# Kernel tuning notes

Hardware: AMD Instinct MI355X
Metric: run time of the kernel (lower is better)

## Reference

```python
import jax, jax.numpy as jnp
import numpy as np

D_MODEL = 1024
N_HEAD = 16
D_HEAD = D_MODEL // N_HEAD


def setup_inputs() -> dict:
    key = jax.random.key(0)
    k_x, k_wqkv, k_bqkv, k_wp, k_bp = jax.random.split(key, 5)
    B, T = 2, 2048
    bound = 1.0 / np.sqrt(D_MODEL)
    return {
        "x": jax.random.normal(k_x, (B, T, D_MODEL), dtype=jnp.float32),
        "w_qkv": jax.random.uniform(k_wqkv, (D_MODEL, 3 * D_MODEL), jnp.float32, -bound, bound),
        "b_qkv": jax.random.uniform(k_bqkv, (3 * D_MODEL,), jnp.float32, -bound, bound),
        "w_proj": jax.random.uniform(k_wp, (D_MODEL, D_MODEL), jnp.float32, -bound, bound),
        "b_proj": jax.random.uniform(k_bp, (D_MODEL,), jnp.float32, -bound, bound),
    }


def reference(x, w_qkv, b_qkv, w_proj, b_proj):
    B, T, C = x.shape
    qkv = x @ w_qkv + b_qkv                       # [B,T,3C]
    qkv = qkv.reshape(B, T, 3, N_HEAD, D_HEAD)
    qkv = jnp.transpose(qkv, (2, 0, 3, 1, 4))      # [3,B,H,T,dh]
    q, k, v = qkv[0], qkv[1], qkv[2]
    scale = np.sqrt(D_HEAD).astype(np.float32)
    attn = jnp.einsum("bhqd,bhkd->bhqk", q, k) / scale  # [B,H,T,T]
    causal = jnp.tril(jnp.ones((T, T), dtype=bool))
    attn = jnp.where(causal, attn, -jnp.inf)
    attn = jax.nn.softmax(attn, axis=-1)
    out = jnp.einsum("bhqk,bhkd->bhqd", attn, v)   # [B,H,T,dh]
    out = jnp.transpose(out, (0, 2, 1, 3)).reshape(B, T, C)
    return out @ w_proj + b_proj
```

## Files before the change

### kernel.cpp

```cpp
#include <hip/hip_runtime.h>
#include <hip/hip_bf16.h>
#include <math.h>

constexpr int Bb   = 2;
constexpr int T    = 2048;
constexpr int C    = 1024;
constexpr int H    = 16;
constexpr int M    = Bb * T;
constexpr int NQKV = 3 * C;

typedef __attribute__((ext_vector_type(8))) short bf16x8;
typedef __attribute__((ext_vector_type(4))) float f32x4;

__device__ inline short f2bf(float f) {
    __hip_bfloat16 h = __float2bfloat16(f);
    return *reinterpret_cast<short*>(&h);
}

#if __has_builtin(__builtin_amdgcn_exp2f)
#define EXP2(x) __builtin_amdgcn_exp2f(x)
#else
#define EXP2(x) exp2f(x)
#endif

#define GLOBAL_AS __attribute__((address_space(1)))
#define LDS_AS    __attribute__((address_space(3)))

__device__ __forceinline__ void gload_lds16(const short* g, short* s) {
    __builtin_amdgcn_global_load_lds((const GLOBAL_AS void*)g, (LDS_AS void*)s, 16, 0, 0);
}

__global__ __launch_bounds__(256)
void prep_all(const float* __restrict__ x, short* __restrict__ xb,
              const float* __restrict__ w_qkv, short* __restrict__ wqkvt,
              const float* __restrict__ w_proj, short* __restrict__ wprojt)
{
    __shared__ float tile[32][33];
    const int blk = blockIdx.x;
    const int tid = threadIdx.x;

    if (blk < 4096) {
        const int i = blk * 1024 + tid * 4;
        const float4 v = *(const float4*)(x + i);
        short4 s;
        s.x = f2bf(v.x); s.y = f2bf(v.y); s.z = f2bf(v.z); s.w = f2bf(v.w);
        *(short4*)(xb + i) = s;
        return;
    }

    const bool isqkv = (blk < 7168);
    const int bidx = isqkv ? (blk - 4096) : (blk - 7168);
    const int nblk = isqkv ? 96 : 32;
    const int N    = isqkv ? NQKV : C;
    const float* W = isqkv ? w_qkv : w_proj;
    short* Wt      = isqkv ? wqkvt : wprojt;

    const int n0 = (bidx % nblk) * 32, k0 = (bidx / nblk) * 32;
    const int tx = tid & 31, ty = tid >> 5;
#pragma unroll
    for (int i = 0; i < 32; i += 8)
        tile[ty + i][tx] = W[(size_t)(k0 + ty + i) * N + n0 + tx];
    __syncthreads();
#pragma unroll
    for (int i = 0; i < 32; i += 8)
        Wt[(size_t)(n0 + ty + i) * C + k0 + tx] = f2bf(tile[tx][ty + i]);
}

__global__ __launch_bounds__(256)
void gemm_mfma(const short* __restrict__ A, const short* __restrict__ Bt,
               const float* __restrict__ bias, short* __restrict__ outp,
               int Ndim, int Kdim)
{
    __shared__ __align__(16) short As[2 * 128 * 32];
    __shared__ __align__(16) short Bs[2 * 128 * 32];

    const int tid = threadIdx.x;
    const int w   = tid >> 6;
    const int l   = tid & 63;
    const int lk  = l & 15;
    const int lq  = l >> 4;

    const int gx  = gridDim.x;
    const int nwg = gx * gridDim.y;
    const int cpx = nwg >> 3;
    const int bid = blockIdx.y * gx + blockIdx.x;
    const int swz = (bid & 7) * cpx + (bid >> 3);
    const int m0  = (swz / gx) * 128;
    const int n0  = (swz % gx) * 128;

    const int mw  = (w >> 1) * 64, nw = (w & 1) * 64;

    const int srow = w * 16 + (l >> 2);
    const int scol = (l & 3) * 8;

    const short* agp0 = A  + (size_t)(m0 + srow)      * Kdim + scol;
    const short* agp1 = A  + (size_t)(m0 + 64 + srow) * Kdim + scol;
    const short* bgp0 = Bt + (size_t)(n0 + srow)      * Kdim + scol;
    const short* bgp1 = Bt + (size_t)(n0 + 64 + srow) * Kdim + scol;

    short* ad0 = &As[w * 512];
    short* ad1 = &As[2048 + w * 512];
    short* bd0 = &Bs[w * 512];
    short* bd1 = &Bs[2048 + w * 512];

    f32x4 acc[4][4];
#pragma unroll
    for (int i = 0; i < 4; ++i)
#pragma unroll
        for (int j = 0; j < 4; ++j) acc[i][j] = (f32x4){0.f, 0.f, 0.f, 0.f};

    gload_lds16(agp0, ad0);
    gload_lds16(agp1, ad1);
    gload_lds16(bgp0, bd0);
    gload_lds16(bgp1, bd1);
    __syncthreads();

    int cur = 0;
    for (int k0 = 0; k0 < Kdim; k0 += 32) {
        const int coff = cur ? 4096 : 0;

        bf16x8 af[4], bfr[4];
#pragma unroll
        for (int mt = 0; mt < 4; ++mt)
            af[mt] = *(const bf16x8*)&As[coff + (mw + mt * 16 + lk) * 32 + lq * 8];
#pragma unroll
        for (int nt = 0; nt < 4; ++nt)
            bfr[nt] = *(const bf16x8*)&Bs[coff + (nw + nt * 16 + lk) * 32 + lq * 8];

        if (k0 + 32 < Kdim) {
            const int noff = cur ? 0 : 4096;
            gload_lds16(agp0 + k0 + 32, ad0 + noff);
            gload_lds16(agp1 + k0 + 32, ad1 + noff);
            gload_lds16(bgp0 + k0 + 32, bd0 + noff);
            gload_lds16(bgp1 + k0 + 32, bd1 + noff);
        }

#pragma unroll
        for (int mt = 0; mt < 4; ++mt)
#pragma unroll
            for (int nt = 0; nt < 4; ++nt)
                acc[mt][nt] = __builtin_amdgcn_mfma_f32_16x16x32_bf16(bfr[nt], af[mt], acc[mt][nt], 0, 0, 0);

        __syncthreads();
        cur ^= 1;
    }

    float4 bv[4];
#pragma unroll
    for (int nt = 0; nt < 4; ++nt)
        bv[nt] = *(const float4*)(bias + n0 + nw + nt * 16 + lq * 4);
#pragma unroll
    for (int mt = 0; mt < 4; ++mt) {
        short* rowp = outp + (size_t)(m0 + mw + mt * 16 + lk) * Ndim + n0 + nw + lq * 4;
#pragma unroll
        for (int nt = 0; nt < 4; ++nt) {
            short4 pk;
            pk.x = f2bf(acc[mt][nt][0] + bv[nt].x);
            pk.y = f2bf(acc[mt][nt][1] + bv[nt].y);
            pk.z = f2bf(acc[mt][nt][2] + bv[nt].z);
            pk.w = f2bf(acc[mt][nt][3] + bv[nt].w);
            *(short4*)(rowp + nt * 16) = pk;
        }
    }
}

__global__ __launch_bounds__(256)
void gemm_mfma_proj(const short* __restrict__ A, const short* __restrict__ Bt,
                    const float* __restrict__ bias, float* __restrict__ outp,
                    int Ndim, int Kdim)
{
    __shared__ __align__(16) short As[2 * 64 * 32];
    __shared__ __align__(16) short Bs[2 * 128 * 32];

    const int tid = threadIdx.x;
    const int w   = tid >> 6;
    const int l   = tid & 63;
    const int lk  = l & 15;
    const int lq  = l >> 4;

    const int gx  = gridDim.x;
    const int nwg = gx * gridDim.y;
    const int cpx = nwg >> 3;
    const int bid = blockIdx.y * gx + blockIdx.x;
    const int swz = (bid & 7) * cpx + (bid >> 3);
    const int m0  = (swz / gx) * 64;
    const int n0  = (swz % gx) * 128;

    const int mw  = (w & 1) * 32, nw = (w >> 1) * 64;

    const int srow = w * 16 + (l >> 2);
    const int scol = (l & 3) * 8;

    const short* agp  = A  + (size_t)(m0 + srow)      * Kdim + scol;
    const short* bgp0 = Bt + (size_t)(n0 + srow)      * Kdim + scol;
    const short* bgp1 = Bt + (size_t)(n0 + 64 + srow) * Kdim + scol;

    short* ad  = &As[w * 512];
    short* bd0 = &Bs[w * 512];
    short* bd1 = &Bs[2048 + w * 512];

    f32x4 acc[2][4];
#pragma unroll
    for (int i = 0; i < 2; ++i)
#pragma unroll
        for (int j = 0; j < 4; ++j) acc[i][j] = (f32x4){0.f, 0.f, 0.f, 0.f};

    gload_lds16(agp,  ad);
    gload_lds16(bgp0, bd0);
    gload_lds16(bgp1, bd1);
    __syncthreads();

    int cur = 0;
    for (int k0 = 0; k0 < Kdim; k0 += 32) {
        const int coffA = cur ? 2048 : 0;
        const int coffB = cur ? 4096 : 0;

        bf16x8 af[2], bfr[4];
#pragma unroll
        for (int mt = 0; mt < 2; ++mt)
            af[mt] = *(const bf16x8*)&As[coffA + (mw + mt * 16 + lk) * 32 + lq * 8];
#pragma unroll
        for (int nt = 0; nt < 4; ++nt)
            bfr[nt] = *(const bf16x8*)&Bs[coffB + (nw + nt * 16 + lk) * 32 + lq * 8];

        if (k0 + 32 < Kdim) {
            const int noffA = cur ? 0 : 2048;
            const int noffB = cur ? 0 : 4096;
            gload_lds16(agp  + k0 + 32, ad  + noffA);
            gload_lds16(bgp0 + k0 + 32, bd0 + noffB);
            gload_lds16(bgp1 + k0 + 32, bd1 + noffB);
        }

#pragma unroll
        for (int mt = 0; mt < 2; ++mt)
#pragma unroll
            for (int nt = 0; nt < 4; ++nt)
                acc[mt][nt] = __builtin_amdgcn_mfma_f32_16x16x32_bf16(bfr[nt], af[mt], acc[mt][nt], 0, 0, 0);

        __syncthreads();
        cur ^= 1;
    }

    float4 bv[4];
#pragma unroll
    for (int nt = 0; nt < 4; ++nt)
        bv[nt] = *(const float4*)(bias + n0 + nw + nt * 16 + lq * 4);
#pragma unroll
    for (int mt = 0; mt < 2; ++mt) {
        float* rowp = outp + (size_t)(m0 + mw + mt * 16 + lk) * Ndim + n0 + nw + lq * 4;
#pragma unroll
        for (int nt = 0; nt < 4; ++nt) {
            float4 v;
            v.x = acc[mt][nt][0] + bv[nt].x;
            v.y = acc[mt][nt][1] + bv[nt].y;
            v.z = acc[mt][nt][2] + bv[nt].z;
            v.w = acc[mt][nt][3] + bv[nt].w;
            *(float4*)(rowp + nt * 16) = v;
        }
    }
}

constexpr int LDV = 136;
constexpr float SC = 0.18033688f;

__global__ __launch_bounds__(256, 4)
void attn_mfma(const short* __restrict__ qkv, short* __restrict__ att)
{
    __shared__ __align__(16) short Ks[128 * 64];
    __shared__ __align__(16) short Vt[64 * LDV];

    const int idx = blockIdx.x;
    const int xcd = idx & 7;
    const int j   = idx >> 3;
    const int bh  = xcd * 4 + (j & 3);
    const int s   = j >> 2;
    const int qt  = (s < 8)  ? (31 - s)
                  : (s < 16) ? (s - 8)
                  : (s < 24) ? (39 - s)
                  :            (s - 16);
    const int b   = bh >> 4;
    const int h   = bh & 15;
    const int qbase = qt * 64;

    const int tid = threadIdx.x;
    const int w   = tid >> 6;
    const int l   = tid & 63;
    const int lk  = l & 15;
    const int lq  = l >> 4;

    const short* base = qkv + (size_t)b * T * 3072 + h * 64;

    const int q_abs = qbase + w * 16 + lk;
    const short* qp = base + (size_t)q_abs * 3072 + lq * 8;
    const bf16x8 qf0 = *(const bf16x8*)qp;
    const bf16x8 qf1 = *(const bf16x8*)(qp + 32);

    f32x4 acc_o[4];
#pragma unroll
    for (int dt = 0; dt < 4; ++dt) acc_o[dt] = (f32x4){0.f, 0.f, 0.f, 0.f};
    float m_run = -INFINITY;
    float l_run = 0.f;

    const int krow   = l >> 3;
    const int kcolsw = 8 * ((l & 7) ^ (l >> 3));
    const int swz    = lk & 7;

    const int kg   = tid & 31;
    const int vd0  = (tid >> 5) * 8;
    const int pcol = ((kg & 24) | ((kg & 3) << 1) | ((kg >> 2) & 1)) * 4;

    const int nkt = (qbase + 64 + 127) >> 7;
#pragma unroll 1
    for (int it = 0; it < nkt; ++it) {
        const int j0 = it * 128;
        __syncthreads();
#pragma unroll
        for (int rr = 0; rr < 4; ++rr) {
            const int g = w * 32 + rr * 8;
            gload_lds16(base + 1024 + (size_t)(j0 + g + krow) * 3072 + kcolsw, &Ks[g * 64]);
        }
        {
            const short* vp = base + 2048 + (size_t)(j0 + kg * 4) * 3072 + vd0;
            bf16x8 vv[4];
#pragma unroll
            for (int kk = 0; kk < 4; ++kk)
                vv[kk] = *(const bf16x8*)(vp + (size_t)kk * 3072);
#pragma unroll
            for (int d = 0; d < 8; ++d) {
                short4 pk;
                pk.x = vv[0][d]; pk.y = vv[1][d]; pk.z = vv[2][d]; pk.w = vv[3][d];
                *(short4*)&Vt[(vd0 + d) * LDV + pcol] = pk;
            }
        }
        __syncthreads();

        f32x4 s4[8];
#pragma unroll
        for (int kt = 0; kt < 8; ++kt) {
            const int row = kt * 16 + lk;
            const bf16x8 kf0 = *(const bf16x8*)&Ks[row * 64 + 8 * (lq ^ swz)];
            const bf16x8 kf1 = *(const bf16x8*)&Ks[row * 64 + 8 * ((lq + 4) ^ swz)];
            f32x4 a = (f32x4){0.f, 0.f, 0.f, 0.f};
            a = __builtin_amdgcn_mfma_f32_16x16x32_bf16(kf0, qf0, a, 0, 0, 0);
            a = __builtin_amdgcn_mfma_f32_16x16x32_bf16(kf1, qf1, a, 0, 0, 0);
            s4[kt] = a;
        }

        if (it == nkt - 1) {
#pragma unroll
            for (int kt = 0; kt < 8; ++kt)
#pragma unroll
                for (int r = 0; r < 4; ++r)
                    if (j0 + kt * 16 + lq * 4 + r > q_abs) s4[kt][r] = -1e30f;
        }

        float mx = s4[0][0];
#pragma unroll
        for (int kt = 0; kt < 8; ++kt)
#pragma unroll
            for (int r = 0; r < 4; ++r) mx = fmaxf(mx, s4[kt][r]);
        mx = fmaxf(mx, __shfl_xor(mx, 16));
        mx = fmaxf(mx, __shfl_xor(mx, 32));
        const float mn   = fmaxf(m_run, mx);
        const float corr = EXP2((m_run - mn) * SC);
        m_run = mn;
        const float nmc = -mn * SC;
#pragma unroll
        for (int kt = 0; kt < 8; ++kt)
#pragma unroll
            for (int r = 0; r < 4; ++r)
                s4[kt][r] = EXP2(fmaf(s4[kt][r], SC, nmc));
        float ps = 0.f;
#pragma unroll
        for (int kt = 0; kt < 8; ++kt)
            ps += ((s4[kt][0] + s4[kt][1]) + (s4[kt][2] + s4[kt][3]));
        ps += __shfl_xor(ps, 16);
        ps += __shfl_xor(ps, 32);
        l_run = l_run * corr + ps;

        unsigned int d0[8], d1[8];
#pragma unroll
        for (int kt = 0; kt < 8; ++kt) {
            d0[kt] = (unsigned int)(unsigned short)f2bf(s4[kt][0])
                   | ((unsigned int)(unsigned short)f2bf(s4[kt][1]) << 16);
            d1[kt] = (unsigned int)(unsigned short)f2bf(s4[kt][2])
                   | ((unsigned int)(unsigned short)f2bf(s4[kt][3]) << 16);
        }

#pragma unroll
        for (int dt = 0; dt < 4; ++dt)
#pragma unroll
            for (int r = 0; r < 4; ++r) acc_o[dt][r] *= corr;

#pragma unroll
        for (int kc = 0; kc < 4; ++kc) {
            union { unsigned int u[4]; bf16x8 v; } up;
            up.u[0] = d0[kc * 2];
            up.u[1] = d1[kc * 2];
            up.u[2] = d0[kc * 2 + 1];
            up.u[3] = d1[kc * 2 + 1];
            const bf16x8 pf = up.v;
#pragma unroll
            for (int dt = 0; dt < 4; ++dt) {
                const bf16x8 vf = *(const bf16x8*)&Vt[(dt * 16 + lk) * LDV + kc * 32 + lq * 8];
                acc_o[dt] = __builtin_amdgcn_mfma_f32_16x16x32_bf16(vf, pf, acc_o[dt], 0, 0, 0);
            }
        }
    }

    const float inv = 1.f / l_run;
    short* op = att + ((size_t)(b * T + q_abs)) * 1024 + h * 64;
#pragma unroll
    for (int dt = 0; dt < 4; ++dt) {
        short4 pk;
        pk.x = f2bf(acc_o[dt][0] * inv);
        pk.y = f2bf(acc_o[dt][1] * inv);
        pk.z = f2bf(acc_o[dt][2] * inv);
        pk.w = f2bf(acc_o[dt][3] * inv);
        *(short4*)(op + dt * 16 + lq * 4) = pk;
    }
}

extern "C" void kernel_launch(void* const* d_in, const int* in_sizes, int n_in,
                              void* d_out, int out_size, void* d_ws, size_t ws_size,
                              hipStream_t stream)
{
    const float* x      = (const float*)d_in[0];
    const float* w_qkv  = (const float*)d_in[1];
    const float* b_qkv  = (const float*)d_in[2];
    const float* w_proj = (const float*)d_in[3];
    const float* b_proj = (const float*)d_in[4];
    float* out = (float*)d_out;

    short* xb     = (short*)d_ws;
    short* wqkvt  = xb     + (size_t)M * C;
    short* wprojt = wqkvt  + (size_t)NQKV * C;
    short* qkvb   = wprojt + (size_t)C * C;
    short* attb   = qkvb   + (size_t)M * NQKV;

    prep_all<<<8192, 256, 0, stream>>>(x, xb, w_qkv, wqkvt, w_proj, wprojt);
    gemm_mfma<<<dim3(NQKV / 128, M / 128), 256, 0, stream>>>(xb, wqkvt, b_qkv, qkvb, NQKV, C);
    attn_mfma<<<1024, 256, 0, stream>>>(qkvb, attb);
    gemm_mfma_proj<<<dim3(C / 128, M / 64), 256, 0, stream>>>(attb, wprojt, b_proj, out, C, C);
}
```

Measured before the change: 179.8 us.

## Double-buffer K/V tiles in attention with 512-thread blocks over 128-query tiles

The attention kernel now uses 512-thread blocks, each covering 128 queries, with double-buffered shared memory for K and transposed V. Warps 0-3 prefetch the next K tile through direct global-to-LDS loads, and warps 4-7 load the next V tile into registers and write it transposed after the PV MFMAs. The aim is to overlap global loads with compute, drop one barrier per iteration, and share each K/V tile across twice as many queries. In exchange, shared memory per block doubles and the grid halves to 512 blocks, which may lower occupancy and load balance under the causal mask.

```diff
diff --git a/kernel.cpp b/kernel.cpp
--- a/kernel.cpp
+++ b/kernel.cpp
@@ -263,24 +263,21 @@
 constexpr int LDV = 136;
 constexpr float SC = 0.18033688f;
 
-__global__ __launch_bounds__(256, 4)
+__global__ __launch_bounds__(512, 4)
 void attn_mfma(const short* __restrict__ qkv, short* __restrict__ att)
 {
-    __shared__ __align__(16) short Ks[128 * 64];
-    __shared__ __align__(16) short Vt[64 * LDV];
+    __shared__ __align__(16) short Ks[2][128 * 64];
+    __shared__ __align__(16) short Vt[2][64 * LDV];
 
     const int idx = blockIdx.x;
     const int xcd = idx & 7;
     const int j   = idx >> 3;
     const int bh  = xcd * 4 + (j & 3);
     const int s   = j >> 2;
-    const int qt  = (s < 8)  ? (31 - s)
-                  : (s < 16) ? (s - 8)
-                  : (s < 24) ? (39 - s)
-                  :            (s - 16);
+    const int qt  = (s < 8) ? s : (23 - s);
     const int b   = bh >> 4;
     const int h   = bh & 15;
-    const int qbase = qt * 64;
+    const int qbase = qt * 128;
 
     const int tid = threadIdx.x;
     const int w   = tid >> 6;
@@ -306,40 +303,62 @@
     const int swz    = lk & 7;
 
     const int kg   = tid & 31;
-    const int vd0  = (tid >> 5) * 8;
+    const int vd0  = ((tid >> 5) & 7) * 8;
     const int pcol = ((kg & 24) | ((kg & 3) << 1) | ((kg >> 2) & 1)) * 4;
 
-    const int nkt = (qbase + 64 + 127) >> 7;
+    const int nkt = qt + 1;
+
+    bf16x8 vv[4];
+
+    if (w < 4) {
+#pragma unroll
+        for (int rr = 0; rr < 4; ++rr) {
+            const int g = w * 32 + rr * 8;
+            gload_lds16(base + 1024 + (size_t)(g + krow) * 3072 + kcolsw, &Ks[0][g * 64]);
+        }
+    } else {
+        const short* vp = base + 2048 + (size_t)(kg * 4) * 3072 + vd0;
+#pragma unroll
+        for (int kk = 0; kk < 4; ++kk)
+            vv[kk] = *(const bf16x8*)(vp + (size_t)kk * 3072);
+#pragma unroll
+        for (int d = 0; d < 8; ++d) {
+            short4 pk;
+            pk.x = vv[0][d]; pk.y = vv[1][d]; pk.z = vv[2][d]; pk.w = vv[3][d];
+            *(short4*)&Vt[0][(vd0 + d) * LDV + pcol] = pk;
+        }
+    }
+    __syncthreads();
+
 #pragma unroll 1
     for (int it = 0; it < nkt; ++it) {
-        const int j0 = it * 128;
-        __syncthreads();
-#pragma unroll
-        for (int rr = 0; rr < 4; ++rr) {
-            const int g = w * 32 + rr * 8;
-            gload_lds16(base + 1024 + (size_t)(j0 + g + krow) * 3072 + kcolsw, &Ks[g * 64]);
-        }
-        {
-            const short* vp = base + 2048 + (size_t)(j0 + kg * 4) * 3072 + vd0;
-            bf16x8 vv[4];
-#pragma unroll
-            for (int kk = 0; kk < 4; ++kk)
-                vv[kk] = *(const bf16x8*)(vp + (size_t)kk * 3072);
-#pragma unroll
-            for (int d = 0; d < 8; ++d) {
-                short4 pk;
-                pk.x = vv[0][d]; pk.y = vv[1][d]; pk.z = vv[2][d]; pk.w = vv[3][d];
-                *(short4*)&Vt[(vd0 + d) * LDV + pcol] = pk;
+        const int j0  = it * 128;
+        const int buf = it & 1;
+        const int nb  = buf ^ 1;
+
+        if (it + 1 < nkt) {
+            const int j1 = j0 + 128;
+            if (w < 4) {
+#pragma unroll
+                for (int rr = 0; rr < 4; ++rr) {
+                    const int g = w * 32 + rr * 8;
+                    gload_lds16(base + 1024 + (size_t)(j1 + g + krow) * 3072 + kcolsw,
+                                &Ks[nb][g * 64]);
+                }
+            } else {
+                const short* vp = base + 2048 + (size_t)(j1 + kg * 4) * 3072 + vd0;
+#pragma unroll
+                for (int kk = 0; kk < 4; ++kk)
+                    vv[kk] = *(const bf16x8*)(vp + (size_t)kk * 3072);
             }
         }
-        __syncthreads();
 
         f32x4 s4[8];
 #pragma unroll
         for (int kt = 0; kt < 8; ++kt) {
             const int row = kt * 16 + lk;
-            const bf16x8 kf0 = *(const bf16x8*)&Ks[row * 64 + 8 * (lq ^ swz)];
-            const bf16x8 kf1 = *(const bf16x8*)&Ks[row * 64 + 8 * ((lq + 4) ^ swz)];
+            const bf16x8 kf0 = *(const bf16x8*)&Ks[buf][row * 64 + 8 * (lq ^ swz)];
+            const bf16x8 kf1 = *(const bf16x8*)&Ks[buf][row * 64 + 8 * ((lq + 4) ^ swz)];
             f32x4 a = (f32x4){0.f, 0.f, 0.f, 0.f};
             a = __builtin_amdgcn_mfma_f32_16x16x32_bf16(kf0, qf0, a, 0, 0, 0);
             a = __builtin_amdgcn_mfma_f32_16x16x32_bf16(kf1, qf1, a, 0, 0, 0);
@@ -402,10 +421,21 @@
             const bf16x8 pf = up.v;
 #pragma unroll
             for (int dt = 0; dt < 4; ++dt) {
-                const bf16x8 vf = *(const bf16x8*)&Vt[(dt * 16 + lk) * LDV + kc * 32 + lq * 8];
+                const bf16x8 vf = *(const bf16x8*)&Vt[buf][(dt * 16 + lk) * LDV + kc * 32 + lq * 8];
                 acc_o[dt] = __builtin_amdgcn_mfma_f32_16x16x32_bf16(vf, pf, acc_o[dt], 0, 0, 0);
             }
         }
+
+        if (it + 1 < nkt && w >= 4) {
+#pragma unroll
+            for (int d = 0; d < 8; ++d) {
+                short4 pk;
+                pk.x = vv[0][d]; pk.y = vv[1][d]; pk.z = vv[2][d]; pk.w = vv[3][d];
+                *(short4*)&Vt[nb][(vd0 + d) * LDV + pcol] = pk;
+            }
+        }
+
+        __syncthreads();
     }
 
     const float inv = 1.f / l_run;
@@ -440,6 +470,6 @@
 
     prep_all<<<8192, 256, 0, stream>>>(x, xb, w_qkv, wqkvt, w_proj, wprojt);
     gemm_mfma<<<dim3(NQKV / 128, M / 128), 256, 0, stream>>>(xb, wqkvt, b_qkv, qkvb, NQKV, C);
-    attn_mfma<<<1024, 256, 0, stream>>>(qkvb, attb);
+    attn_mfma<<<512, 512, 0, stream>>>(qkvb, attb);
     gemm_mfma_proj<<<dim3(C / 128, M / 64), 256, 0, stream>>>(attb, wprojt, b_proj, out, C, C);
 }
```

Measured after the change: 177.6 us. Within noise of the previous version (-1.2%).
